# Performance work log

Hardware: AMD Instinct MI355X
Metric: run time of the kernel (lower is better)

## Reference

```python
import jax, jax.numpy as jnp
import numpy as np

B, NV, NDIRS, NRINGS, NCH, NF = 2, 15000, 16, 3, 32, 64


def setup_inputs() -> dict:
    key = jax.random.key(0)
    k1, k2, k3, k4 = jax.random.split(key, 4)
    y = jax.random.normal(k1, (B, NV, NDIRS, NCH), dtype=jnp.float32)
    ft_v = jax.random.randint(k2, (NV, NRINGS, NDIRS), 0, NV, dtype=jnp.int32)
    ft_d = jax.random.randint(k3, (NV, NRINGS, NDIRS), 0, NDIRS, dtype=jnp.int32)
    kernel = jax.random.normal(k4, (NRINGS, NDIRS, NCH, NF), dtype=jnp.float32) * 0.05
    bias = jnp.zeros((NF,), dtype=jnp.float32)
    return {"y": y, "ft_v": ft_v, "ft_d": ft_d, "kernel": kernel, "bias": bias}


def reference(y, ft_v, ft_d, kernel, bias):
    # y: [b, nv, ndirs, nch]; ft_v/ft_d: [nv, nrings, ndirs]; kernel: [nrings, ndirs, nch, nf]
    b, nv, ndirs, nch = y.shape
    f = jnp.transpose(y, (1, 2, 3, 0))  # [nv, ndirs, nch, b]
    dirs = jnp.arange(ndirs)

    def per_dir(l):
        # cyclic forward shift of the direction axis, composed with the
        # frame-transporter gather: z[v,r,d,c,b] = f[ft_v[v,r,d], (ft_d[v,r,d]+l)%n, c, b]
        d_idx = (ft_d + l) % ndirs                # [nv, nrings, ndirs]
        z = f[ft_v, d_idx]                        # [nv, nrings, ndirs, nch, b]
        # kernel shifted in reverse: k_l[:, d] = kernel[:, (d-l)%n]
        k_l = kernel[:, (dirs - l) % ndirs]       # [nrings, ndirs, nch, nf]
        return jnp.einsum('vrdcb,rdcf->vbf', z, k_l)  # [nv, b, nf]

    out = jax.lax.map(per_dir, dirs)              # [ndirs, nv, b, nf] (sequential, like tf.while_loop)
    out = jnp.transpose(out, (2, 1, 0, 3))        # [b, nv, ndirs, nf]
    out = out + bias
    return jax.nn.relu(out)
```

## Files before the change

### kernel.cpp

```cpp
#include <hip/hip_runtime.h>

#define NV 15000
#define ND 16
#define NR 3
#define NC 32
#define NFDIM 64
#define BB 2

typedef short bf16x8 __attribute__((ext_vector_type(8)));
typedef float f32x4 __attribute__((ext_vector_type(4)));
typedef unsigned short u16x8 __attribute__((ext_vector_type(8)));

#define KB_OFF     30720000u
#define WS_NEEDED  30916608u

__device__ __forceinline__ unsigned short f2bf(float x) {
  union { float f; unsigned int u; } cv; cv.f = x;
  unsigned int u = cv.u;
  u += 0x7FFF + ((u >> 16) & 1);
  return (unsigned short)(u >> 16);
}

__global__ void prep_y(const float* __restrict__ y, u16x8* __restrict__ yt) {
  int tid = blockIdx.x * 256 + threadIdx.x;
  if (tid >= (NV * ND * BB * NC) / 8) return;
  int o   = tid * 8;
  int v   = o >> 10;
  int rem = o & 1023;
  int d   = rem >> 6;
  int b   = (rem >> 5) & 1;
  int c0  = rem & 31;
  const f32x4* src = (const f32x4*)(y + (((b * NV + v) * ND + d) * NC + c0));
  f32x4 lo = src[0], hi = src[1];
  u16x8 r;
#pragma unroll
  for (int i = 0; i < 4; i++) { r[i] = f2bf(lo[i]); r[4 + i] = f2bf(hi[i]); }
  yt[tid] = r;
}

__global__ void prep_kb(const float* __restrict__ kern, unsigned short* __restrict__ kb) {
  int t = blockIdx.x * 256 + threadIdx.x;
  if (t >= 48 * 4 * 64) return;
  int lane  = t & 63;
  int ft    = (t >> 6) & 3;
  int chunk = t >> 8;
  int q = lane >> 4;
  int f = (lane & 15) * 4 + ft;
  unsigned short* dst = kb + t * 8;
#pragma unroll
  for (int j = 0; j < 8; j++) {
    int k = q * 8 + j;
    dst[j] = f2bf(kern[(chunk * NC + k) * NFDIM + f]);
  }
}

__global__ __launch_bounds__(256, 5) void sync_conv_main(
    const unsigned short* __restrict__ yt, const unsigned short* __restrict__ kb,
    const int* __restrict__ ftv, const int* __restrict__ ftd,
    const float* __restrict__ bias, float* __restrict__ out) {
  __shared__ int pidx_lds[16][49];

  int tid  = threadIdx.x;
  int lane = tid & 63;
  int mg   = blockIdx.x >> 2;
  int lg   = blockIdx.x & 3;
  int l    = lg * 4 + (tid >> 6);
  int vbase = mg * 16;

  for (int t = tid; t < 16 * 48; t += 256) {
    int i = t / 48, j = t - i * 48;
    int v = vbase + i; v = v < NV ? v : NV - 1;
    pidx_lds[i][j] = ftv[v * 48 + j] * 16 + (ftd[v * 48 + j] & 15);
  }
  __syncthreads();

  int q    = lane >> 4;
  int n    = lane & 15;
  int b    = n & 1;
  int voff = n >> 1;
  int lane_elem = b * 32 + q * 8;
  const unsigned short* kb_lane = kb + lane * 8;

  f32x4 acc[2][4];
#pragma unroll
  for (int i = 0; i < 2; i++)
#pragma unroll
    for (int j = 0; j < 4; j++) acc[i][j] = (f32x4){0.f, 0.f, 0.f, 0.f};

  for (int r = 0; r < NR; r++) {
#pragma unroll
    for (int dg = 0; dg < 4; dg++) {
      bf16x8 afr[2][4];
#pragma unroll
      for (int mt = 0; mt < 2; mt++)
#pragma unroll
        for (int ds = 0; ds < 4; ds++) {
          int p  = pidx_lds[mt * 8 + voff][r * 16 + dg * 4 + ds];
          int dd = ((p & 15) + l) & 15;
          int off = (p >> 4) * 1024 + (dd << 6) + lane_elem;
          afr[mt][ds] = *reinterpret_cast<const bf16x8*>(yt + off);
        }
#pragma unroll
      for (int ds = 0; ds < 4; ds++) {
        int d  = dg * 4 + ds;
        int dp = (d - l) & 15;
        const unsigned short* kbp = kb_lane + (r * 16 + dp) * 2048;
        bf16x8 bfr[4];
#pragma unroll
        for (int ft = 0; ft < 4; ft++)
          bfr[ft] = *reinterpret_cast<const bf16x8*>(kbp + ft * 512);
#pragma unroll
        for (int mt = 0; mt < 2; mt++)
#pragma unroll
          for (int ft = 0; ft < 4; ft++)
            acc[mt][ft] = __builtin_amdgcn_mfma_f32_16x16x32_bf16(
                afr[mt][ds], bfr[ft], acc[mt][ft], 0, 0, 0);
      }
    }
  }

  f32x4 bv = *reinterpret_cast<const f32x4*>(bias + 4 * n);

#pragma unroll
  for (int mt = 0; mt < 2; mt++) {
#pragma unroll
    for (int reg = 0; reg < 4; reg++) {
      int m  = q * 4 + reg;
      int v  = vbase + mt * 8 + (m >> 1);
      int bb = m & 1;
      if (v < NV) {
        f32x4 x;
#pragma unroll
        for (int ft = 0; ft < 4; ft++) {
          float t = acc[mt][ft][reg] + bv[ft];
          x[ft] = t > 0.f ? t : 0.f;
        }
        float* dst = out + (((bb * NV + v) * ND + l) * NFDIM) + 4 * n;
        __builtin_nontemporal_store(x, (f32x4*)dst);
      }
    }
  }
}

__global__ void fallback_kernel(const float* __restrict__ y, const int* __restrict__ ftv,
                                const int* __restrict__ ftd, const float* __restrict__ kern,
                                const float* __restrict__ bias, float* __restrict__ out) {
  int idx = blockIdx.x;
  int l = idx & 15;
  int v = (idx >> 4) % NV;
  int b = idx / (NV * ND);
  int f = threadIdx.x;
  float acc = 0.f;
  for (int r = 0; r < NR; r++)
    for (int d = 0; d < ND; d++) {
      int ii = (v * NR + r) * ND + d;
      int vv = ftv[ii];
      int dd = (ftd[ii] + l) & 15;
      int dp = (d - l) & 15;
      const float* yp = y + ((b * NV + vv) * ND + dd) * NC;
      const float* kp = kern + ((r * 16 + dp) * NC) * NFDIM + f;
#pragma unroll 8
      for (int c = 0; c < NC; c++) acc += yp[c] * kp[c * NFDIM];
    }
  float x = acc + bias[f];
  out[idx * NFDIM + f] = x > 0.f ? x : 0.f;
}

extern "C" void kernel_launch(void* const* d_in, const int* in_sizes, int n_in,
                              void* d_out, int out_size, void* d_ws, size_t ws_size,
                              hipStream_t stream) {
  const float* y    = (const float*)d_in[0];
  const int*   ftv  = (const int*)d_in[1];
  const int*   ftd  = (const int*)d_in[2];
  const float* kern = (const float*)d_in[3];
  const float* bias = (const float*)d_in[4];
  float* out = (float*)d_out;

  if (ws_size >= (size_t)WS_NEEDED) {
    char* ws = (char*)d_ws;
    unsigned short* yt = (unsigned short*)ws;
    unsigned short* kb = (unsigned short*)(ws + KB_OFF);

    prep_y<<<(NV * ND * BB * NC / 8 + 255) / 256, 256, 0, stream>>>(y, (u16x8*)yt);
    prep_kb<<<(48 * 4 * 64 + 255) / 256, 256, 0, stream>>>(kern, kb);
    sync_conv_main<<<3752, 256, 0, stream>>>(yt, kb, ftv, ftd, bias, out);
  } else {
    fallback_kernel<<<BB * NV * ND, NFDIM, 0, stream>>>(y, ftv, ftd, kern, bias, out);
  }
}
```

Baseline: 388.1 us.

## Software-pipeline gathers and kernel loads with double-buffered register batches

Replaces the ring/direction-group loop with a flat 48-step loop in batches of two directions. Each batch's gathered y fragments and kernel fragments are loaded into one of two register buffers while the MFMAs consume the other, so global-load latency overlaps with matrix math. The launch-bounds occupancy hint drops from 5 to 3 to leave room for the extra live registers, which reduces the number of waves available to hide latency.

```diff
diff --git a/kernel.cpp b/kernel.cpp
--- a/kernel.cpp
+++ b/kernel.cpp
@@ -54,7 +54,7 @@
   }
 }
 
-__global__ __launch_bounds__(256, 5) void sync_conv_main(
+__global__ __launch_bounds__(256, 3) void sync_conv_main(
     const unsigned short* __restrict__ yt, const unsigned short* __restrict__ kb,
     const int* __restrict__ ftv, const int* __restrict__ ftd,
     const float* __restrict__ bias, float* __restrict__ out) {
@@ -87,36 +87,46 @@
 #pragma unroll
     for (int j = 0; j < 4; j++) acc[i][j] = (f32x4){0.f, 0.f, 0.f, 0.f};
 
-  for (int r = 0; r < NR; r++) {
-#pragma unroll
-    for (int dg = 0; dg < 4; dg++) {
-      bf16x8 afr[2][4];
-#pragma unroll
-      for (int mt = 0; mt < 2; mt++)
-#pragma unroll
-        for (int ds = 0; ds < 4; ds++) {
-          int p  = pidx_lds[mt * 8 + voff][r * 16 + dg * 4 + ds];
-          int dd = ((p & 15) + l) & 15;
-          int off = (p >> 4) * 1024 + (dd << 6) + lane_elem;
-          afr[mt][ds] = *reinterpret_cast<const bf16x8*>(yt + off);
-        }
-#pragma unroll
-      for (int ds = 0; ds < 4; ds++) {
-        int d  = dg * 4 + ds;
-        int dp = (d - l) & 15;
-        const unsigned short* kbp = kb_lane + (r * 16 + dp) * 2048;
-        bf16x8 bfr[4];
-#pragma unroll
-        for (int ft = 0; ft < 4; ft++)
-          bfr[ft] = *reinterpret_cast<const bf16x8*>(kbp + ft * 512);
-#pragma unroll
-        for (int mt = 0; mt < 2; mt++)
-#pragma unroll
-          for (int ft = 0; ft < 4; ft++)
-            acc[mt][ft] = __builtin_amdgcn_mfma_f32_16x16x32_bf16(
-                afr[mt][ds], bfr[ft], acc[mt][ft], 0, 0, 0);
+  bf16x8 bufA[2][2][2];
+  bf16x8 bufB[2][2][4];
+
+  auto load_batch = [&](int bidx, int par) {
+    int k0 = bidx * 2;
+#pragma unroll
+    for (int ds = 0; ds < 2; ds++) {
+      int k = k0 + ds;
+      int r = k >> 4;
+      int dp = ((k & 15) - l) & 15;
+      const unsigned short* kbp = kb_lane + (r * 16 + dp) * 2048;
+#pragma unroll
+      for (int ft = 0; ft < 4; ft++)
+        bufB[par][ds][ft] = *reinterpret_cast<const bf16x8*>(kbp + ft * 512);
+#pragma unroll
+      for (int mt = 0; mt < 2; mt++) {
+        int p  = pidx_lds[mt * 8 + voff][k];
+        int dd = ((p & 15) + l) & 15;
+        int off = (p >> 4) * 1024 + (dd << 6) + lane_elem;
+        bufA[par][mt][ds] = *reinterpret_cast<const bf16x8*>(yt + off);
       }
     }
+  };
+  auto compute_batch = [&](int par) {
+#pragma unroll
+    for (int ds = 0; ds < 2; ds++)
+#pragma unroll
+      for (int mt = 0; mt < 2; mt++)
+#pragma unroll
+        for (int ft = 0; ft < 4; ft++)
+          acc[mt][ft] = __builtin_amdgcn_mfma_f32_16x16x32_bf16(
+              bufA[par][mt][ds], bufB[par][ds][ft], acc[mt][ft], 0, 0, 0);
+  };
+
+  load_batch(0, 0);
+  for (int i = 0; i < 12; i++) {
+    load_batch(2 * i + 1, 1);
+    compute_batch(0);
+    if (i < 11) load_batch(2 * i + 2, 0);
+    compute_batch(1);
   }
 
   f32x4 bv = *reinterpret_cast<const f32x4*>(bias + 4 * n);
```

Result: faster. 376.1 us (-3.1%).
